# Performance work log

Measured on AMD Instinct MI355X. Metric: run time of the kernel, lower is better.

Reference implementation:

```python
import jax, jax.numpy as jnp
import numpy as np
import math

B, S, D, NH, HFF, E, K, C, L, V = 8, 256, 1024, 16, 2048, 8, 2, 10, 4, 32000
HD = D // NH
EPS = 1e-5


def _pos_encoding(max_len, d_model):
    pos = jnp.arange(max_len, dtype=jnp.float32)[:, None]
    div = jnp.exp(jnp.arange(0, d_model, 2, dtype=jnp.float32) * (-math.log(10000.0) / d_model))
    pe = jnp.zeros((max_len, d_model), dtype=jnp.float32)
    pe = pe.at[:, 0::2].set(jnp.sin(pos * div))
    pe = pe.at[:, 1::2].set(jnp.cos(pos * div))
    return pe[:, None, :]  # [max_len, 1, D], matching torch buffer layout


def _layernorm(x, g, b):
    mu = jnp.mean(x, axis=-1, keepdims=True)
    var = jnp.mean((x - mu) ** 2, axis=-1, keepdims=True)
    return (x - mu) * jax.lax.rsqrt(var + EPS) * g + b


def setup_inputs() -> dict:
    key = jax.random.key(0)
    ks = jax.random.split(key, 20)
    sc = lambda *shape: 0.02
    inp = {
        "src": jax.random.randint(ks[0], (B, S), 0, V, dtype=jnp.int32),
        "emb": jax.random.normal(ks[1], (V, D), jnp.float32) * 0.02,
        "in_proj_w": jax.random.normal(ks[2], (L, 3 * D, D), jnp.float32) * 0.02,
        "in_proj_b": jnp.zeros((L, 3 * D), jnp.float32),
        "out_w": jax.random.normal(ks[3], (L, D, D), jnp.float32) * 0.02,
        "out_b": jnp.zeros((L, D), jnp.float32),
        "ln1_g": jnp.ones((L, D), jnp.float32),
        "ln1_b": jnp.zeros((L, D), jnp.float32),
        "ln2_g": jnp.ones((L, D), jnp.float32),
        "ln2_b": jnp.zeros((L, D), jnp.float32),
        "gate_w": jax.random.normal(ks[4], (L, E, D), jnp.float32) * 0.02,
        "gate_b": jnp.zeros((L, E), jnp.float32),
        "w1": jax.random.normal(ks[5], (L, E, D, HFF), jnp.float32) * 0.02,
        "b1": jnp.zeros((L, E, HFF), jnp.float32),
        "w2": jax.random.normal(ks[6], (L, E, HFF, D), jnp.float32) * 0.02,
        "b2": jnp.zeros((L, E, D), jnp.float32),
        "cls_w": jax.random.normal(ks[7], (C, D), jnp.float32) * 0.02,
        "cls_b": jnp.zeros((C,), jnp.float32),
    }
    return inp


def _attention(x, ipw, ipb, ow, ob):
    # x: [B,S,D]
    qkv = x @ ipw.T + ipb  # [B,S,3D]
    q, k, v = jnp.split(qkv, 3, axis=-1)
    q = q.reshape(B, S, NH, HD)
    k = k.reshape(B, S, NH, HD)
    v = v.reshape(B, S, NH, HD)
    scores = jnp.einsum("bqhd,bkhd->bhqk", q, k) / math.sqrt(HD)
    attn = jax.nn.softmax(scores, axis=-1)
    o = jnp.einsum("bhqk,bkhd->bqhd", attn, v).reshape(B, S, D)
    return o @ ow.T + ob


def _moe(x, gw, gb, w1, b1, w2, b2):
    # x: [B,S,D]; gw: [E,D]; w1: [E,D,H]; w2: [E,H,D]
    t = x.reshape(B * S, D)
    logits = t @ gw.T + gb  # [T,E]
    topv, topi = jax.lax.top_k(logits, K)  # [T,K]
    weights = jax.nn.softmax(topv, axis=-1)  # [T,K]
    # dense expert compute (small E, compute-bound), combine via top-k gather
    h = jax.nn.relu(jnp.einsum("td,edh->teh", t, w1) + b1)  # [T,E,H]
    y = jnp.einsum("teh,ehd->ted", h, w2) + b2  # [T,E,D]
    sel = jnp.take_along_axis(y, topi[:, :, None], axis=1)  # [T,K,D]
    out = jnp.sum(sel * weights[:, :, None], axis=1)  # [T,D]
    return out.reshape(B, S, D), logits.reshape(B, S, E)


def reference(src, emb, in_proj_w, in_proj_b, out_w, out_b, ln1_g, ln1_b,
              ln2_g, ln2_b, gate_w, gate_b, w1, b1, w2, b2, cls_w, cls_b):
    x = emb[src] * math.sqrt(D)  # [B,S,D]
    pe = _pos_encoding(5000, D)  # [max_len,1,D]
    # faithful to original: pe indexed by batch dim (x.size(0)), broadcast over seq
    x = x + pe[:B]  # [B,1,D] -> broadcast [B,S,D]
    all_gates = []
    for l in range(in_proj_w.shape[0]):
        a = _attention(x, in_proj_w[l], in_proj_b[l], out_w[l], out_b[l])
        x = _layernorm(x + a, ln1_g[l], ln1_b[l])
        m, g = _moe(x, gate_w[l], gate_b[l], w1[l], b1[l], w2[l], b2[l])
        x = _layernorm(x + m, ln2_g[l], ln2_b[l])
        all_gates.append(g)
    pooled = jnp.mean(x, axis=1)  # [B,D]
    out = pooled @ cls_w.T + cls_b  # [B,C]
    return out, jnp.stack(all_gates)  # ([B,C], [L,B,S,E])
```

## Files before the change

### kernel.cpp

```cpp
#include <hip/hip_runtime.h>
#include <math.h>

#define TKN 2048
#define DIM 1024
#define NHEAD 16
#define HDIM 64
#define HFF 2048
#define NE 8
#define TOPK 2
#define NCLS 10
#define NLAYER 4
#define SEQ 256
#define BATCH 8

typedef __attribute__((ext_vector_type(8))) _Float16 f16x8;
typedef __attribute__((ext_vector_type(4))) float f32x4;
typedef __attribute__((ext_vector_type(16))) float f32x16;
typedef __attribute__((ext_vector_type(8))) unsigned short u16x8;

__device__ __forceinline__ unsigned short f2h(float v) {
  _Float16 h = (_Float16)v;
  return __builtin_bit_cast(unsigned short, h);
}
__device__ __forceinline__ void fsplit(float v, unsigned short& hi, unsigned short& lo) {
  _Float16 h = (_Float16)v;
  hi = __builtin_bit_cast(unsigned short, h);
  lo = f2h(v - (float)h);
}
__device__ __forceinline__ void split8(float4 f0, float4 f1, f16x8& h, f16x8& l) {
  float fv[8] = {f0.x, f0.y, f0.z, f0.w, f1.x, f1.y, f1.z, f1.w};
#pragma unroll
  for (int i = 0; i < 8; ++i) {
    _Float16 hh = (_Float16)fv[i];
    h[i] = hh;
    l[i] = (_Float16)(fv[i] - (float)hh);
  }
}

__device__ __forceinline__ void gload_lds16(const void* g, void* l) {
  __builtin_amdgcn_global_load_lds((__attribute__((address_space(1))) void*)g,
                                   (__attribute__((address_space(3))) void*)l,
                                   16, 0, 0);
}

__global__ __launch_bounds__(256) void k_embed(const int* __restrict__ src,
                                               const float* __restrict__ emb,
                                               float* __restrict__ x,
                                               unsigned short* __restrict__ xhi,
                                               unsigned short* __restrict__ xlo) {
  const int t = blockIdx.x;
  const int tid = threadIdx.x;
  const int b = t / SEQ;
  const int tok = src[t];
  const float* erow = emb + (size_t)tok * DIM;
  const size_t base = (size_t)t * DIM;
  const float cexp = -9.210340371976184f / 1024.0f;
#pragma unroll
  for (int j = 0; j < 4; ++j) {
    int d = tid + 256 * j;
    int i2 = d & ~1;
    float ang = (float)b * expf((float)i2 * cexp);
    float pe = (d & 1) ? cosf(ang) : sinf(ang);
    float v = erow[d] * 32.0f + pe;
    x[base + d] = v;
    fsplit(v, xhi[base + d], xlo[base + d]);
  }
}

template <bool LO>
__global__ __launch_bounds__(256) void k_cvt_split(const float* __restrict__ in,
                                                   unsigned short* __restrict__ ohi,
                                                   unsigned short* __restrict__ olo) {
  int i = blockIdx.x * 256 + threadIdx.x;
  float4 v = ((const float4*)in)[i];
  ushort4 h, l;
  fsplit(v.x, h.x, l.x); fsplit(v.y, h.y, l.y);
  fsplit(v.z, h.z, l.z); fsplit(v.w, h.w, l.w);
  ((ushort4*)ohi)[i] = h;
  if (LO) ((ushort4*)olo)[i] = l;
}

template <bool LO>
__global__ __launch_bounds__(256) void k_cvt_t2(const float* __restrict__ in,
                                                unsigned short* __restrict__ ohi,
                                                unsigned short* __restrict__ olo,
                                                int R, int Cc) {
  __shared__ float ts[64][33];
  const int t = threadIdx.x;
  const int c0 = blockIdx.x * 32, r0 = blockIdx.y * 64;
  const float* ip = in + (size_t)blockIdx.z * R * Cc;
  const size_t obase = (size_t)blockIdx.z * R * Cc;
  const int cc = t & 31, rr0 = t >> 5;
#pragma unroll
  for (int j = 0; j < 8; ++j)
    ts[rr0 + 8 * j][cc] = ip[(size_t)(r0 + rr0 + 8 * j) * Cc + c0 + cc];
  __syncthreads();
  const int c = t >> 3, rch = (t & 7) * 8;
  u16x8 hv, lv;
#pragma unroll
  for (int i = 0; i < 8; ++i) {
    unsigned short hi, lo;
    fsplit(ts[rch + i][c], hi, lo);
    hv[i] = hi; lv[i] = lo;
  }
  size_t o = obase + (size_t)(c0 + c) * R + r0 + rch;
  *(u16x8*)(ohi + o) = hv;
  if (LO) *(u16x8*)(olo + o) = lv;
}

template <int MODE, bool RELU, int OUTK, bool SPLIT>
__global__ __launch_bounds__(256) void k_mfma_gemm(
    const unsigned short* __restrict__ Ahi, const unsigned short* __restrict__ Alo,
    const unsigned short* __restrict__ Bhi, const unsigned short* __restrict__ Blo,
    const float* __restrict__ bias, void* __restrict__ out0, void* __restrict__ out1,
    int M, int N, int K,
    const int* __restrict__ slot_token, const int* __restrict__ offg) {
  constexpr int NP = SPLIT ? 2 : 1;
  __shared__ unsigned short U[2][NP][128 * 64];
  const int tid = threadIdx.x;
  const int w = tid >> 6, lane = tid & 63;
  const int bm = blockIdx.y * 128, bn = blockIdx.x * 128;
  int r0 = 0, rows = M, e = 0;
  if (MODE != 0) {
    e = blockIdx.z;
    r0 = offg[e];
    rows = offg[e + 1] - r0;
    if (bm >= rows) return;
  }
  const size_t bwb = (size_t)e * K * N;
  const float* biasq = bias + (size_t)e * N;

  const int lrow8 = lane >> 3;
  const int s = (lane & 7) ^ lrow8;
  const int chunk = (s & 3) * 8;
  const unsigned short* sp0[4];
  const unsigned short* sp1[4];
#pragma unroll
  for (int i = 0; i < 4; ++i) {
    int rloc = w * 32 + i * 8 + lrow8;
    int growA;
    if (MODE == 0) {
      growA = bm + rloc;
    } else {
      int rr = bm + rloc;
      if (rr >= rows) rr = rows - 1;
      growA = (MODE == 1) ? slot_token[r0 + rr] : (r0 + rr);
    }
    size_t aoff = (size_t)growA * K + chunk;
    size_t boff = bwb + (size_t)(bn + rloc) * K + chunk;
    if constexpr (SPLIT) {
      sp0[i] = (s < 4 ? Ahi : Alo) + aoff;
      sp1[i] = (s < 4 ? Bhi : Blo) + boff;
    } else {
      sp0[i] = (s < 4) ? (Ahi + aoff) : (Bhi + boff);
      sp1[i] = nullptr;
    }
  }

  f32x16 acc[2][2] = {};
  const int wr = w >> 1, wc = w & 1;
  const int l31 = lane & 31, kq = lane >> 5;
  const int sw = lane & 7;
  unsigned aof[2][2], bof[2][2];
#pragma unroll
  for (int mt = 0; mt < 2; ++mt)
#pragma unroll
    for (int kh = 0; kh < 2; ++kh)
      aof[mt][kh] = (unsigned)((wr * 64 + mt * 32 + l31) * 64 + (((kh * 2 + kq) ^ sw) * 8));
#pragma unroll
  for (int nt = 0; nt < 2; ++nt)
#pragma unroll
    for (int kh = 0; kh < 2; ++kh)
      bof[nt][kh] = (unsigned)((wc * 64 + nt * 32 + l31) * 64 + (((kh * 2 + kq) ^ sw) * 8));

#pragma unroll
  for (int i = 0; i < 4; ++i) {
    gload_lds16(sp0[i], &U[0][0][(w * 32 + i * 8) * 64]);
    sp0[i] += 32;
    if constexpr (SPLIT) {
      gload_lds16(sp1[i], &U[0][1][(w * 32 + i * 8) * 64]);
      sp1[i] += 32;
    }
  }

  const int NT = K / 32;
#pragma unroll 2
  for (int t = 0; t < NT; ++t) {
    const int cur = t & 1;
    if (t + 1 < NT) {
#pragma unroll
      for (int i = 0; i < 4; ++i) {
        gload_lds16(sp0[i], &U[cur ^ 1][0][(w * 32 + i * 8) * 64]);
        sp0[i] += 32;
        if constexpr (SPLIT) {
          gload_lds16(sp1[i], &U[cur ^ 1][1][(w * 32 + i * 8) * 64]);
          sp1[i] += 32;
        }
      }
      if constexpr (SPLIT)
        asm volatile("s_waitcnt vmcnt(8)" ::: "memory");
      else
        asm volatile("s_waitcnt vmcnt(4)" ::: "memory");
    } else {
      asm volatile("s_waitcnt vmcnt(0)" ::: "memory");
    }
    __builtin_amdgcn_s_barrier();

    f16x8 Ah[2][2], Bh[2][2], Al[2][2], Bl[2][2];
#pragma unroll
    for (int mt = 0; mt < 2; ++mt)
#pragma unroll
      for (int kh = 0; kh < 2; ++kh) {
        Ah[mt][kh] = *(const f16x8*)&U[cur][0][aof[mt][kh]];
        if constexpr (SPLIT) Al[mt][kh] = *(const f16x8*)&U[cur][0][aof[mt][kh] ^ 32];
      }
#pragma unroll
    for (int nt = 0; nt < 2; ++nt)
#pragma unroll
      for (int kh = 0; kh < 2; ++kh) {
        if constexpr (SPLIT) {
          Bh[nt][kh] = *(const f16x8*)&U[cur][1][bof[nt][kh]];
          Bl[nt][kh] = *(const f16x8*)&U[cur][1][bof[nt][kh] ^ 32];
        } else {
          Bh[nt][kh] = *(const f16x8*)&U[cur][0][bof[nt][kh] ^ 32];
        }
      }
#pragma unroll
    for (int mt = 0; mt < 2; ++mt)
#pragma unroll
      for (int nt = 0; nt < 2; ++nt)
#pragma unroll
        for (int kh = 0; kh < 2; ++kh) {
          acc[mt][nt] = __builtin_amdgcn_mfma_f32_32x32x16_f16(Ah[mt][kh], Bh[nt][kh], acc[mt][nt], 0, 0, 0);
          if constexpr (SPLIT) {
            acc[mt][nt] = __builtin_amdgcn_mfma_f32_32x32x16_f16(Ah[mt][kh], Bl[nt][kh], acc[mt][nt], 0, 0, 0);
            acc[mt][nt] = __builtin_amdgcn_mfma_f32_32x32x16_f16(Al[mt][kh], Bh[nt][kh], acc[mt][nt], 0, 0, 0);
          }
        }
    __builtin_amdgcn_s_barrier();
  }

  float bv[2];
#pragma unroll
  for (int nt = 0; nt < 2; ++nt) bv[nt] = biasq[bn + wc * 64 + nt * 32 + l31];

#pragma unroll
  for (int mt = 0; mt < 2; ++mt) {
#pragma unroll
    for (int reg = 0; reg < 16; ++reg) {
      int rloc = (reg & 3) + 8 * (reg >> 2) + 4 * kq;
      int rowg = bm + wr * 64 + mt * 32 + rloc;
      if (MODE != 0 && rowg >= rows) continue;
      size_t crow = (size_t)((MODE == 0) ? rowg : (r0 + rowg)) * N;
#pragma unroll
      for (int nt = 0; nt < 2; ++nt) {
        float v = acc[mt][nt][reg] + bv[nt];
        if (RELU) v = fmaxf(v, 0.f);
        size_t o = crow + bn + wc * 64 + nt * 32 + l31;
        if (OUTK == 0) {
          ((float*)out0)[o] = v;
        } else if (OUTK == 1) {
          ((unsigned short*)out0)[o] = f2h(v);
        } else {
          unsigned short hi, lo;
          fsplit(v, hi, lo);
          ((unsigned short*)out0)[o] = hi;
          ((unsigned short*)out1)[o] = lo;
        }
      }
    }
  }
}

__global__ __launch_bounds__(256) void k_attn(const float* __restrict__ qkv,
                                              unsigned short* __restrict__ ohi,
                                              unsigned short* __restrict__ olo) {
  __shared__ float ps[16][256];
  const int qt = blockIdx.x, hh = blockIdx.y, bb = blockIdx.z;
  const int tid = threadIdx.x, w = tid >> 6, lane = tid & 63;
  const int lr = lane & 15, lg = lane >> 4;
  const int t0 = bb * SEQ + qt * 16;

  f16x8 qh[2], ql[2];
#pragma unroll
  for (int kh = 0; kh < 2; ++kh) {
    const float* qb = qkv + (size_t)(t0 + lr) * (3 * DIM) + hh * 64 + kh * 32 + lg * 8;
    split8(*(const float4*)qb, *(const float4*)(qb + 4), qh[kh], ql[kh]);
  }
#pragma unroll
  for (int nt = 0; nt < 4; ++nt) {
    f16x8 kvh[2], kvl[2];
#pragma unroll
    for (int kh = 0; kh < 2; ++kh) {
      const float* kb = qkv + (size_t)(bb * SEQ + w * 64 + nt * 16 + lr) * (3 * DIM)
                        + DIM + hh * 64 + kh * 32 + lg * 8;
      split8(*(const float4*)kb, *(const float4*)(kb + 4), kvh[kh], kvl[kh]);
    }
    f32x4 a = {0.f, 0.f, 0.f, 0.f};
#pragma unroll
    for (int kh = 0; kh < 2; ++kh) {
      a = __builtin_amdgcn_mfma_f32_16x16x32_f16(qh[kh], kvh[kh], a, 0, 0, 0);
// ... 41 lines not shown
    }
  }
  float accs[4] = {a0, a1, a2, a3};
#pragma unroll
  for (int j = 0; j < 4; ++j) {
    size_t o = (size_t)(t0 + qi0 + 4 * j) * DIM + hh * 64 + d;
    fsplit(accs[j], ohi[o], olo[o]);
  }
}

__device__ __forceinline__ float block_reduce_sum(float v, float* red) {
  const int tid = threadIdx.x;
  red[tid] = v;
  __syncthreads();
  for (int s = 128; s > 0; s >>= 1) {
    if (tid < s) red[tid] += red[tid + s];
    __syncthreads();
  }
  float r = red[0];
  __syncthreads();
  return r;
}

__global__ __launch_bounds__(256) void k_add_ln_gate(const float* __restrict__ xin,
                                                     const float* __restrict__ add,
                                                     const float* __restrict__ g,
                                                     const float* __restrict__ bt,
                                                     const float* __restrict__ gw,
                                                     const float* __restrict__ gb,
                                                     float* __restrict__ xout,
                                                     unsigned short* __restrict__ xhi,
                                                     unsigned short* __restrict__ xlo,
                                                     float* __restrict__ gout,
                                                     int* __restrict__ topi,
                                                     float* __restrict__ topw) {
  __shared__ float red[256];
  __shared__ float pw[4][NE];
  __shared__ float lgs[NE];
  const int t = blockIdx.x, tid = threadIdx.x;
  const size_t base = (size_t)t * DIM;
  float v[4];
  float s = 0.f;
#pragma unroll
  for (int j = 0; j < 4; ++j) {
    int d = tid + 256 * j;
    v[j] = xin[base + d] + add[base + d];
    s += v[j];
  }
  float mean = block_reduce_sum(s, red) * (1.0f / DIM);
  float s2 = 0.f;
#pragma unroll
  for (int j = 0; j < 4; ++j) { float dv = v[j] - mean; s2 += dv * dv; }
  float var = block_reduce_sum(s2, red) * (1.0f / DIM);
  float rs = rsqrtf(var + 1e-5f);
  float o[4];
#pragma unroll
  for (int j = 0; j < 4; ++j) {
    int d = tid + 256 * j;
    o[j] = (v[j] - mean) * rs * g[d] + bt[d];
    xout[base + d] = o[j];
    fsplit(o[j], xhi[base + d], xlo[base + d]);
  }
  const int wv = tid >> 6, lane = tid & 63;
  float p[NE];
#pragma unroll
  for (int e = 0; e < NE; ++e) {
    float pe = 0.f;
#pragma unroll
    for (int j = 0; j < 4; ++j) pe += o[j] * gw[(size_t)e * DIM + tid + 256 * j];
    for (int m = 32; m; m >>= 1) pe += __shfl_xor(pe, m);
    p[e] = pe;
  }
  if (lane == 0) {
#pragma unroll
    for (int e = 0; e < NE; ++e) pw[wv][e] = p[e];
  }
  __syncthreads();
  if (tid < NE) {
    float l = pw[0][tid] + pw[1][tid] + pw[2][tid] + pw[3][tid] + gb[tid];
    gout[(size_t)t * NE + tid] = l;
    lgs[tid] = l;
  }
  __syncthreads();
  if (tid == 0) {
    int i0 = 0; float v0 = lgs[0];
    for (int i = 1; i < NE; ++i) if (lgs[i] > v0) { v0 = lgs[i]; i0 = i; }
    int i1 = -1; float v1 = -1e30f;
    for (int i = 0; i < NE; ++i) { if (i == i0) continue; if (lgs[i] > v1) { v1 = lgs[i]; i1 = i; } }
    float e1 = expf(v1 - v0);
    float w0 = 1.0f / (1.0f + e1);
    topi[2 * t] = i0; topi[2 * t + 1] = i1;
    topw[2 * t] = w0; topw[2 * t + 1] = e1 * w0;
  }
}

__global__ __launch_bounds__(512) void k_route(const int* __restrict__ topi,
                                               int* __restrict__ offg,
                                               int* __restrict__ slot_token,
                                               int* __restrict__ slot_of) {
  __shared__ int cnt_s[NE];
  __shared__ int off_s[NE + 1];
  const int tid = threadIdx.x;
  const int w = tid >> 6, lane = tid & 63;
  int c = 0;
  for (int i = lane; i < TKN * TOPK; i += 64) c += (topi[i] == w) ? 1 : 0;
  for (int m = 32; m; m >>= 1) c += __shfl_xor(c, m);
  if (lane == 0) cnt_s[w] = c;
  __syncthreads();
  if (tid == 0) {
    off_s[0] = 0;
    for (int e2 = 0; e2 < NE; ++e2) off_s[e2 + 1] = off_s[e2] + cnt_s[e2];
    for (int e2 = 0; e2 <= NE; ++e2) offg[e2] = off_s[e2];
  }
  __syncthreads();
  int base = off_s[w];
  for (int i0 = 0; i0 < TKN * TOPK; i0 += 64) {
    int i = i0 + lane;
    bool mm = (topi[i] == w);
    unsigned long long mask = __ballot(mm ? 1 : 0);
    int rank = __popcll(mask & ((1ull << lane) - 1ull));
    if (mm) {
      int slot = base + rank;
      slot_token[slot] = i >> 1;
      slot_of[i] = slot;
    }
    base += __popcll(mask);
  }
}

__global__ __launch_bounds__(256) void k_moe_combine_ln(const float* __restrict__ xin,
                                                        const float* __restrict__ y,
                                                        const float* __restrict__ topw,
                                                        const int* __restrict__ slot_of,
                                                        const float* __restrict__ g,
                                                        const float* __restrict__ bt,
                                                        float* __restrict__ xout,
                                                        unsigned short* __restrict__ xhi,
                                                        unsigned short* __restrict__ xlo) {
  __shared__ float red[256];
  const int t = blockIdx.x, tid = threadIdx.x;
  const float w0 = topw[2 * t], w1v = topw[2 * t + 1];
  const int s0 = slot_of[2 * t], s1 = slot_of[2 * t + 1];
  const size_t base = (size_t)t * DIM;
  float v[4];
  float s = 0.f;
#pragma unroll
  for (int j = 0; j < 4; ++j) {
    int d = tid + 256 * j;
    v[j] = xin[base + d] + w0 * y[(size_t)s0 * DIM + d] + w1v * y[(size_t)s1 * DIM + d];
    s += v[j];
  }
  float mean = block_reduce_sum(s, red) * (1.0f / DIM);
  float s2 = 0.f;
#pragma unroll
  for (int j = 0; j < 4; ++j) { float dv = v[j] - mean; s2 += dv * dv; }
  float var = block_reduce_sum(s2, red) * (1.0f / DIM);
  float rs = rsqrtf(var + 1e-5f);
#pragma unroll
  for (int j = 0; j < 4; ++j) {
// ... 28 lines not shown
  }
}

extern "C" void kernel_launch(void* const* d_in, const int* in_sizes, int n_in,
                              void* d_out, int out_size, void* d_ws, size_t ws_size,
                              hipStream_t stream) {
  const int*   src  = (const int*)  d_in[0];
  const float* emb  = (const float*)d_in[1];
  const float* ipw  = (const float*)d_in[2];
  const float* ipb  = (const float*)d_in[3];
  const float* ow   = (const float*)d_in[4];
  const float* ob   = (const float*)d_in[5];
  const float* ln1g = (const float*)d_in[6];
  const float* ln1b = (const float*)d_in[7];
  const float* ln2g = (const float*)d_in[8];
  const float* ln2b = (const float*)d_in[9];
  const float* gw   = (const float*)d_in[10];
  const float* gb   = (const float*)d_in[11];
  const float* w1   = (const float*)d_in[12];
  const float* b1   = (const float*)d_in[13];
  const float* w2   = (const float*)d_in[14];
  const float* b2   = (const float*)d_in[15];
  const float* cw   = (const float*)d_in[16];
  const float* cb   = (const float*)d_in[17];
  float* out = (float*)d_out;

  char* ws = (char*)d_ws;
  size_t off = 0;
  auto carve = [&](size_t bytes) -> void* {
    void* p = ws + off;
    off += (bytes + 255) & ~(size_t)255;
    return p;
  };
  float*          x     = (float*)carve((size_t)TKN * DIM * 4);
  unsigned short* xhi   = (unsigned short*)carve((size_t)TKN * DIM * 2);
  unsigned short* xlo   = (unsigned short*)carve((size_t)TKN * DIM * 2);
  char*           bufQ  = (char*)carve((size_t)2 * TKN * TOPK * HFF * 2);
  float*          qkv   = (float*)bufQ;
  unsigned short* h_hi  = (unsigned short*)bufQ;
  unsigned short* h_lo  = (unsigned short*)(bufQ + (size_t)TKN * TOPK * HFF * 2);
  unsigned short* at_hi = (unsigned short*)carve((size_t)TKN * DIM * 2);
  unsigned short* at_lo = (unsigned short*)carve((size_t)TKN * DIM * 2);
  char*           bufP  = (char*)carve((size_t)TKN * TOPK * DIM * 4);
  float*          proj  = (float*)bufP;
  float*          ybuf  = (float*)bufP;
  unsigned short* wq_hi = (unsigned short*)carve((size_t)3 * DIM * DIM * 2);
  unsigned short* wq_lo = (unsigned short*)carve((size_t)3 * DIM * DIM * 2);
  unsigned short* wo_hi = (unsigned short*)carve((size_t)DIM * DIM * 2);
  unsigned short* wo_lo = (unsigned short*)carve((size_t)DIM * DIM * 2);
  unsigned short* wt_hi = (unsigned short*)carve((size_t)NE * DIM * HFF * 2);
  unsigned short* wt_lo = (unsigned short*)carve((size_t)NE * DIM * HFF * 2);
  float* topw       = (float*)carve((size_t)TKN * TOPK * 4);
  int*   topi       = (int*)  carve((size_t)TKN * TOPK * 4);
  int*   slot_token = (int*)  carve((size_t)TKN * TOPK * 4);
  int*   slot_of    = (int*)  carve((size_t)TKN * TOPK * 4);
  int*   offg       = (int*)  carve(64);

  k_embed<<<TKN, 256, 0, stream>>>(src, emb, x, xhi, xlo);

  for (int l = 0; l < NLAYER; ++l) {
    const float* ipw_l = ipw + (size_t)l * 3 * DIM * DIM;
    const float* ow_l  = ow  + (size_t)l * DIM * DIM;
    const float* w1_l  = w1  + (size_t)l * NE * DIM * HFF;
    const float* w2_l  = w2  + (size_t)l * NE * HFF * DIM;
    const bool spd = (l < 3);
    const bool spm = (l < 2);

    if (spd) {
      k_cvt_split<true><<<(3 * DIM * DIM) / 1024, 256, 0, stream>>>(ipw_l, wq_hi, wq_lo);
      k_cvt_split<true><<<(DIM * DIM) / 1024, 256, 0, stream>>>(ow_l, wo_hi, wo_lo);
    } else {
      k_cvt_split<false><<<(3 * DIM * DIM) / 1024, 256, 0, stream>>>(ipw_l, wq_hi, wq_lo);
      k_cvt_split<false><<<(DIM * DIM) / 1024, 256, 0, stream>>>(ow_l, wo_hi, wo_lo);
    }
    if (spm)
      k_cvt_t2<true><<<dim3(HFF / 32, DIM / 64, NE), 256, 0, stream>>>(w1_l, wt_hi, wt_lo, DIM, HFF);
    else
      k_cvt_t2<false><<<dim3(HFF / 32, DIM / 64, NE), 256, 0, stream>>>(w1_l, wt_hi, wt_lo, DIM, HFF);

    if (spd)
      k_mfma_gemm<0, false, 0, true><<<dim3(3 * DIM / 128, TKN / 128), 256, 0, stream>>>(
          xhi, xlo, wq_hi, wq_lo, ipb + (size_t)l * 3 * DIM, qkv, nullptr, TKN, 3 * DIM, DIM, nullptr, nullptr);
    else
      k_mfma_gemm<0, false, 0, false><<<dim3(3 * DIM / 128, TKN / 128), 256, 0, stream>>>(
          xhi, xlo, wq_hi, wq_lo, ipb + (size_t)l * 3 * DIM, qkv, nullptr, TKN, 3 * DIM, DIM, nullptr, nullptr);

    k_attn<<<dim3(SEQ / 16, NHEAD, BATCH), 256, 0, stream>>>(qkv, at_hi, at_lo);

    if (spd)
      k_mfma_gemm<0, false, 0, true><<<dim3(DIM / 128, TKN / 128), 256, 0, stream>>>(
          at_hi, at_lo, wo_hi, wo_lo, ob + (size_t)l * DIM, proj, nullptr, TKN, DIM, DIM, nullptr, nullptr);
    else
      k_mfma_gemm<0, false, 0, false><<<dim3(DIM / 128, TKN / 128), 256, 0, stream>>>(
          at_hi, at_lo, wo_hi, wo_lo, ob + (size_t)l * DIM, proj, nullptr, TKN, DIM, DIM, nullptr, nullptr);

    k_add_ln_gate<<<TKN, 256, 0, stream>>>(x, proj, ln1g + l * DIM, ln1b + l * DIM,
                                           gw + (size_t)l * NE * DIM, gb + l * NE,
                                           x, xhi, xlo,
                                           out + NCLS * BATCH + (size_t)l * TKN * NE, topi, topw);
    k_route<<<1, 512, 0, stream>>>(topi, offg, slot_token, slot_of);

    if (spm)
      k_mfma_gemm<1, true, 2, true><<<dim3(HFF / 128, TKN * TOPK / 128, NE), 256, 0, stream>>>(
          xhi, xlo, wt_hi, wt_lo, b1 + (size_t)l * NE * HFF, h_hi, h_lo, 0, HFF, DIM, slot_token, offg);
    else
      k_mfma_gemm<1, true, 1, false><<<dim3(HFF / 128, TKN * TOPK / 128, NE), 256, 0, stream>>>(
          xhi, xlo, wt_hi, wt_lo, b1 + (size_t)l * NE * HFF, h_hi, nullptr, 0, HFF, DIM, slot_token, offg);

    if (spm)
      k_cvt_t2<true><<<dim3(DIM / 32, HFF / 64, NE), 256, 0, stream>>>(w2_l, wt_hi, wt_lo, HFF, DIM);
    else
      k_cvt_t2<false><<<dim3(DIM / 32, HFF / 64, NE), 256, 0, stream>>>(w2_l, wt_hi, wt_lo, HFF, DIM);

    if (spm)
      k_mfma_gemm<2, false, 0, true><<<dim3(DIM / 128, TKN * TOPK / 128, NE), 256, 0, stream>>>(
          h_hi, h_lo, wt_hi, wt_lo, b2 + (size_t)l * NE * DIM, ybuf, nullptr, 0, DIM, HFF, nullptr, offg);
    else
      k_mfma_gemm<2, false, 0, false><<<dim3(DIM / 128, TKN * TOPK / 128, NE), 256, 0, stream>>>(
          h_hi, h_lo, wt_hi, wt_lo, b2 + (size_t)l * NE * DIM, ybuf, nullptr, 0, DIM, HFF, nullptr, offg);

    k_moe_combine_ln<<<TKN, 256, 0, stream>>>(x, ybuf, topw, slot_of,
                                              ln2g + l * DIM, ln2b + l * DIM, x, xhi, xlo);
  }
  k_pool_cls<<<BATCH, 256, 0, stream>>>(x, cw, cb, out);
}
```

Measured before the change: 1.447 ms.

## Split MFMA GEMM tile across eight waves and merge weight conversion launches

The 128x128 MFMA GEMM block now runs 512 threads (8 waves), with each wave computing a 64x32 sub-tile instead of 64x64. Global-to-LDS loading and the wait counts are rebalanced to match. The aim is to cut per-wave accumulator registers and get more waves per CU to hide memory and LDS latency. In exchange, each wave reuses fragments less, so LDS reads per MFMA rise, and every k-step barrier now has to sync more waves. Separately, the two QKV and output-projection weight conversion kernels are fused into one launch with an index split.

```diff
diff --git a/kernel.cpp b/kernel.cpp
--- a/kernel.cpp
+++ b/kernel.cpp
@@ -68,16 +68,25 @@
 }
 
 template <bool LO>
-__global__ __launch_bounds__(256) void k_cvt_split(const float* __restrict__ in,
-                                                   unsigned short* __restrict__ ohi,
-                                                   unsigned short* __restrict__ olo) {
+__global__ __launch_bounds__(256) void k_cvt_split2(const float* __restrict__ inA,
+                                                    unsigned short* __restrict__ hA,
+                                                    unsigned short* __restrict__ lA,
+                                                    int n4A,
+                                                    const float* __restrict__ inB,
+                                                    unsigned short* __restrict__ hB,
+                                                    unsigned short* __restrict__ lB) {
   int i = blockIdx.x * 256 + threadIdx.x;
-  float4 v = ((const float4*)in)[i];
+  const float* in;
+  unsigned short *oh, *ol;
+  int j;
+  if (i < n4A) { in = inA; oh = hA; ol = lA; j = i; }
+  else         { in = inB; oh = hB; ol = lB; j = i - n4A; }
+  float4 v = ((const float4*)in)[j];
   ushort4 h, l;
   fsplit(v.x, h.x, l.x); fsplit(v.y, h.y, l.y);
   fsplit(v.z, h.z, l.z); fsplit(v.w, h.w, l.w);
-  ((ushort4*)ohi)[i] = h;
-  if (LO) ((ushort4*)olo)[i] = l;
+  ((ushort4*)oh)[j] = h;
+  if (LO) ((ushort4*)ol)[j] = l;
 }
 
 template <bool LO>
@@ -109,7 +118,7 @@
 }
 
 template <int MODE, bool RELU, int OUTK, bool SPLIT>
-__global__ __launch_bounds__(256) void k_mfma_gemm(
+__global__ __launch_bounds__(512, 4) void k_mfma_gemm(
     const unsigned short* __restrict__ Ahi, const unsigned short* __restrict__ Alo,
     const unsigned short* __restrict__ Bhi, const unsigned short* __restrict__ Blo,
     const float* __restrict__ bias, void* __restrict__ out0, void* __restrict__ out1,
@@ -133,11 +142,11 @@
   const int lrow8 = lane >> 3;
   const int s = (lane & 7) ^ lrow8;
   const int chunk = (s & 3) * 8;
-  const unsigned short* sp0[4];
-  const unsigned short* sp1[4];
-#pragma unroll
-  for (int i = 0; i < 4; ++i) {
-    int rloc = w * 32 + i * 8 + lrow8;
+  const unsigned short* sp0[2];
+  const unsigned short* sp1[2];
+#pragma unroll
+  for (int i = 0; i < 2; ++i) {
+    int rloc = w * 16 + i * 8 + lrow8;
     int growA;
     if (MODE == 0) {
       growA = bm + rloc;
@@ -157,28 +166,26 @@
     }
   }
 
-  f32x16 acc[2][2] = {};
-  const int wr = w >> 1, wc = w & 1;
+  f32x16 acc[2] = {};
+  const int wr = w >> 2, wc = w & 3;
   const int l31 = lane & 31, kq = lane >> 5;
-  const int sw = lane & 7;
-  unsigned aof[2][2], bof[2][2];
+  const int sw = l31 & 7;
+  unsigned aof[2][2], bof[2];
 #pragma unroll
   for (int mt = 0; mt < 2; ++mt)
 #pragma unroll
     for (int kh = 0; kh < 2; ++kh)
       aof[mt][kh] = (unsigned)((wr * 64 + mt * 32 + l31) * 64 + (((kh * 2 + kq) ^ sw) * 8));
 #pragma unroll
-  for (int nt = 0; nt < 2; ++nt)
-#pragma unroll
-    for (int kh = 0; kh < 2; ++kh)
-      bof[nt][kh] = (unsigned)((wc * 64 + nt * 32 + l31) * 64 + (((kh * 2 + kq) ^ sw) * 8));
-
-#pragma unroll
-  for (int i = 0; i < 4; ++i) {
-    gload_lds16(sp0[i], &U[0][0][(w * 32 + i * 8) * 64]);
+  for (int kh = 0; kh < 2; ++kh)
+    bof[kh] = (unsigned)((wc * 32 + l31) * 64 + (((kh * 2 + kq) ^ sw) * 8));
+
+#pragma unroll
+  for (int i = 0; i < 2; ++i) {
+    gload_lds16(sp0[i], &U[0][0][(w * 16 + i * 8) * 64]);
     sp0[i] += 32;
     if constexpr (SPLIT) {
-      gload_lds16(sp1[i], &U[0][1][(w * 32 + i * 8) * 64]);
+      gload_lds16(sp1[i], &U[0][1][(w * 16 + i * 8) * 64]);
       sp1[i] += 32;
     }
   }
@@ -189,61 +196,48 @@
     const int cur = t & 1;
     if (t + 1 < NT) {
 #pragma unroll
-      for (int i = 0; i < 4; ++i) {
-        gload_lds16(sp0[i], &U[cur ^ 1][0][(w * 32 + i * 8) * 64]);
+      for (int i = 0; i < 2; ++i) {
+        gload_lds16(sp0[i], &U[cur ^ 1][0][(w * 16 + i * 8) * 64]);
         sp0[i] += 32;
         if constexpr (SPLIT) {
-          gload_lds16(sp1[i], &U[cur ^ 1][1][(w * 32 + i * 8) * 64]);
+          gload_lds16(sp1[i], &U[cur ^ 1][1][(w * 16 + i * 8) * 64]);
           sp1[i] += 32;
         }
       }
       if constexpr (SPLIT)
-        asm volatile("s_waitcnt vmcnt(8)" ::: "memory");
+        asm volatile("s_waitcnt vmcnt(4)" ::: "memory");
       else
-        asm volatile("s_waitcnt vmcnt(4)" ::: "memory");
+        asm volatile("s_waitcnt vmcnt(2)" ::: "memory");
     } else {
       asm volatile("s_waitcnt vmcnt(0)" ::: "memory");
     }
     __builtin_amdgcn_s_barrier();
 
-    f16x8 Ah[2][2], Bh[2][2], Al[2][2], Bl[2][2];
-#pragma unroll
-    for (int mt = 0; mt < 2; ++mt)
-#pragma unroll
-      for (int kh = 0; kh < 2; ++kh) {
-        Ah[mt][kh] = *(const f16x8*)&U[cur][0][aof[mt][kh]];
-        if constexpr (SPLIT) Al[mt][kh] = *(const f16x8*)&U[cur][0][aof[mt][kh] ^ 32];
+#pragma unroll
+    for (int kh = 0; kh < 2; ++kh) {
+      f16x8 Ah0 = *(const f16x8*)&U[cur][0][aof[0][kh]];
+      f16x8 Ah1 = *(const f16x8*)&U[cur][0][aof[1][kh]];
+      if constexpr (SPLIT) {
+        f16x8 Bhv = *(const f16x8*)&U[cur][1][bof[kh]];
+        f16x8 Al0 = *(const f16x8*)&U[cur][0][aof[0][kh] ^ 32];
+        f16x8 Al1 = *(const f16x8*)&U[cur][0][aof[1][kh] ^ 32];
+        f16x8 Blv = *(const f16x8*)&U[cur][1][bof[kh] ^ 32];
+        acc[0] = __builtin_amdgcn_mfma_f32_32x32x16_f16(Ah0, Bhv, acc[0], 0, 0, 0);
+        acc[0] = __builtin_amdgcn_mfma_f32_32x32x16_f16(Ah0, Blv, acc[0], 0, 0, 0);
+        acc[0] = __builtin_amdgcn_mfma_f32_32x32x16_f16(Al0, Bhv, acc[0], 0, 0, 0);
+        acc[1] = __builtin_amdgcn_mfma_f32_32x32x16_f16(Ah1, Bhv, acc[1], 0, 0, 0);
+        acc[1] = __builtin_amdgcn_mfma_f32_32x32x16_f16(Ah1, Blv, acc[1], 0, 0, 0);
+        acc[1] = __builtin_amdgcn_mfma_f32_32x32x16_f16(Al1, Bhv, acc[1], 0, 0, 0);
+      } else {
+        f16x8 Bhv = *(const f16x8*)&U[cur][0][bof[kh] ^ 32];
+        acc[0] = __builtin_amdgcn_mfma_f32_32x32x16_f16(Ah0, Bhv, acc[0], 0, 0, 0);
+        acc[1] = __builtin_amdgcn_mfma_f32_32x32x16_f16(Ah1, Bhv, acc[1], 0, 0, 0);
       }
-#pragma unroll
-    for (int nt = 0; nt < 2; ++nt)
-#pragma unroll
-      for (int kh = 0; kh < 2; ++kh) {
-        if constexpr (SPLIT) {
-          Bh[nt][kh] = *(const f16x8*)&U[cur][1][bof[nt][kh]];
-          Bl[nt][kh] = *(const f16x8*)&U[cur][1][bof[nt][kh] ^ 32];
-        } else {
-          Bh[nt][kh] = *(const f16x8*)&U[cur][0][bof[nt][kh] ^ 32];
-        }
-      }
-#pragma unroll
-    for (int mt = 0; mt < 2; ++mt)
-#pragma unroll
-      for (int nt = 0; nt < 2; ++nt)
-#pragma unroll
-        for (int kh = 0; kh < 2; ++kh) {
-          acc[mt][nt] = __builtin_amdgcn_mfma_f32_32x32x16_f16(Ah[mt][kh], Bh[nt][kh], acc[mt][nt], 0, 0, 0);
-          if constexpr (SPLIT) {
-            acc[mt][nt] = __builtin_amdgcn_mfma_f32_32x32x16_f16(Ah[mt][kh], Bl[nt][kh], acc[mt][nt], 0, 0, 0);
-            acc[mt][nt] = __builtin_amdgcn_mfma_f32_32x32x16_f16(Al[mt][kh], Bh[nt][kh], acc[mt][nt], 0, 0, 0);
-          }
-        }
+    }
     __builtin_amdgcn_s_barrier();
   }
 
-  float bv[2];
-#pragma unroll
-  for (int nt = 0; nt < 2; ++nt) bv[nt] = biasq[bn + wc * 64 + nt * 32 + l31];
-
+  const float bv = biasq[bn + wc * 32 + l31];
 #pragma unroll
   for (int mt = 0; mt < 2; ++mt) {
 #pragma unroll
@@ -252,21 +246,18 @@
       int rowg = bm + wr * 64 + mt * 32 + rloc;
       if (MODE != 0 && rowg >= rows) continue;
       size_t crow = (size_t)((MODE == 0) ? rowg : (r0 + rowg)) * N;
-#pragma unroll
-      for (int nt = 0; nt < 2; ++nt) {
-        float v = acc[mt][nt][reg] + bv[nt];
-        if (RELU) v = fmaxf(v, 0.f);
-        size_t o = crow + bn + wc * 64 + nt * 32 + l31;
-        if (OUTK == 0) {
-          ((float*)out0)[o] = v;
-        } else if (OUTK == 1) {
-          ((unsigned short*)out0)[o] = f2h(v);
-        } else {
-          unsigned short hi, lo;
-          fsplit(v, hi, lo);
-          ((unsigned short*)out0)[o] = hi;
-          ((unsigned short*)out1)[o] = lo;
-        }
+      float v = acc[mt][reg] + bv;
+      if (RELU) v = fmaxf(v, 0.f);
+      size_t o = crow + bn + wc * 32 + l31;
+      if (OUTK == 0) {
+        ((float*)out0)[o] = v;
+      } else if (OUTK == 1) {
+        ((unsigned short*)out0)[o] = f2h(v);
+      } else {
+        unsigned short hi, lo;
+        fsplit(v, hi, lo);
+        ((unsigned short*)out0)[o] = hi;
+        ((unsigned short*)out1)[o] = lo;
       }
     }
   }
@@ -587,6 +578,8 @@
 
   k_embed<<<TKN, 256, 0, stream>>>(src, emb, x, xhi, xlo);
 
+  const int n4wq = 3 * DIM * DIM / 4;
+
   for (int l = 0; l < NLAYER; ++l) {
     const float* ipw_l = ipw + (size_t)l * 3 * DIM * DIM;
     const float* ow_l  = ow  + (size_t)l * DIM * DIM;
@@ -595,32 +588,31 @@
     const bool spd = (l < 3);
     const bool spm = (l < 2);
 
-    if (spd) {
-      k_cvt_split<true><<<(3 * DIM * DIM) / 1024, 256, 0, stream>>>(ipw_l, wq_hi, wq_lo);
-      k_cvt_split<true><<<(DIM * DIM) / 1024, 256, 0, stream>>>(ow_l, wo_hi, wo_lo);
-    } else {
-      k_cvt_split<false><<<(3 * DIM * DIM) / 1024, 256, 0, stream>>>(ipw_l, wq_hi, wq_lo);
-      k_cvt_split<false><<<(DIM * DIM) / 1024, 256, 0, stream>>>(ow_l, wo_hi, wo_lo);
-    }
+    if (spd)
+      k_cvt_split2<true><<<(4 * DIM * DIM) / 1024, 256, 0, stream>>>(
+          ipw_l, wq_hi, wq_lo, n4wq, ow_l, wo_hi, wo_lo);
+    else
+      k_cvt_split2<false><<<(4 * DIM * DIM) / 1024, 256, 0, stream>>>(
+          ipw_l, wq_hi, wq_lo, n4wq, ow_l, wo_hi, wo_lo);
     if (spm)
       k_cvt_t2<true><<<dim3(HFF / 32, DIM / 64, NE), 256, 0, stream>>>(w1_l, wt_hi, wt_lo, DIM, HFF);
     else
       k_cvt_t2<false><<<dim3(HFF / 32, DIM / 64, NE), 256, 0, stream>>>(w1_l, wt_hi, wt_lo, DIM, HFF);
 
     if (spd)
-      k_mfma_gemm<0, false, 0, true><<<dim3(3 * DIM / 128, TKN / 128), 256, 0, stream>>>(
+      k_mfma_gemm<0, false, 0, true><<<dim3(3 * DIM / 128, TKN / 128), 512, 0, stream>>>(
           xhi, xlo, wq_hi, wq_lo, ipb + (size_t)l * 3 * DIM, qkv, nullptr, TKN, 3 * DIM, DIM, nullptr, nullptr);
     else
-      k_mfma_gemm<0, false, 0, false><<<dim3(3 * DIM / 128, TKN / 128), 256, 0, stream>>>(
+      k_mfma_gemm<0, false, 0, false><<<dim3(3 * DIM / 128, TKN / 128), 512, 0, stream>>>(
           xhi, xlo, wq_hi, wq_lo, ipb + (size_t)l * 3 * DIM, qkv, nullptr, TKN, 3 * DIM, DIM, nullptr, nullptr);
 
     k_attn<<<dim3(SEQ / 16, NHEAD, BATCH), 256, 0, stream>>>(qkv, at_hi, at_lo);
 
     if (spd)
-      k_mfma_gemm<0, false, 0, true><<<dim3(DIM / 128, TKN / 128), 256, 0, stream>>>(
+      k_mfma_gemm<0, false, 0, true><<<dim3(DIM / 128, TKN / 128), 512, 0, stream>>>(
           at_hi, at_lo, wo_hi, wo_lo, ob + (size_t)l * DIM, proj, nullptr, TKN, DIM, DIM, nullptr, nullptr);
     else
-      k_mfma_gemm<0, false, 0, false><<<dim3(DIM / 128, TKN / 128), 256, 0, stream>>>(
+      k_mfma_gemm<0, false, 0, false><<<dim3(DIM / 128, TKN / 128), 512, 0, stream>>>(
           at_hi, at_lo, wo_hi, wo_lo, ob + (size_t)l * DIM, proj, nullptr, TKN, DIM, DIM, nullptr, nullptr);
 
     k_add_ln_gate<<<TKN, 256, 0, stream>>>(x, proj, ln1g + l * DIM, ln1b + l * DIM,
@@ -630,10 +622,10 @@
     k_route<<<1, 512, 0, stream>>>(topi, offg, slot_token, slot_of);
 
     if (spm)
-      k_mfma_gemm<1, true, 2, true><<<dim3(HFF / 128, TKN * TOPK / 128, NE), 256, 0, stream>>>(
+      k_mfma_gemm<1, true, 2, true><<<dim3(HFF / 128, TKN * TOPK / 128, NE), 512, 0, stream>>>(
           xhi, xlo, wt_hi, wt_lo, b1 + (size_t)l * NE * HFF, h_hi, h_lo, 0, HFF, DIM, slot_token, offg);
     else
-      k_mfma_gemm<1, true, 1, false><<<dim3(HFF / 128, TKN * TOPK / 128, NE), 256, 0, stream>>>(
+      k_mfma_gemm<1, true, 1, false><<<dim3(HFF / 128, TKN * TOPK / 128, NE), 512, 0, stream>>>(
           xhi, xlo, wt_hi, wt_lo, b1 + (size_t)l * NE * HFF, h_hi, nullptr, 0, HFF, DIM, slot_token, offg);
 
     if (spm)
@@ -642,10 +634,10 @@
       k_cvt_t2<false><<<dim3(DIM / 32, HFF / 64, NE), 256, 0, stream>>>(w2_l, wt_hi, wt_lo, HFF, DIM);
 
     if (spm)
-      k_mfma_gemm<2, false, 0, true><<<dim3(DIM / 128, TKN * TOPK / 128, NE), 256, 0, stream>>>(
+      k_mfma_gemm<2, false, 0, true><<<dim3(DIM / 128, TKN * TOPK / 128, NE), 512, 0, stream>>>(
           h_hi, h_lo, wt_hi, wt_lo, b2 + (size_t)l * NE * DIM, ybuf, nullptr, 0, DIM, HFF, nullptr, offg);
     else
-      k_mfma_gemm<2, false, 0, false><<<dim3(DIM / 128, TKN * TOPK / 128, NE), 256, 0, stream>>>(
+      k_mfma_gemm<2, false, 0, false><<<dim3(DIM / 128, TKN * TOPK / 128, NE), 512, 0, stream>>>(
           h_hi, h_lo, wt_hi, wt_lo, b2 + (size_t)l * NE * DIM, ybuf, nullptr, 0, DIM, HFF, nullptr, offg);
 
     k_moe_combine_ln<<<TKN, 256, 0, stream>>>(x, ybuf, topw, slot_of,
```

New measurement: 1.483 ms. 2.5% more time.

## Replace route kernel with atomic slot assignment and merge weight conversion launches

Applied to the files above, without the earlier changes.

The single-block routing kernel is removed. The gate kernel now claims expert slots directly with atomicAdd into fixed-capacity per-expert regions, and the counters are zeroed in the embed kernel. The qkv/out weight conversions and the w1/w2 transpose conversions are each merged into one launch, with separate buffers so w2 no longer waits on the first expert GEMM. This cuts the kernel launch count and removes a serial one-block routing step. In exchange, slot order becomes nondeterministic, buffers grow to NE*CAP, and the expert grids launch more blocks that exit early.

```diff
diff --git a/kernel.cpp b/kernel.cpp
--- a/kernel.cpp
+++ b/kernel.cpp
@@ -12,6 +12,7 @@
 #define NLAYER 4
 #define SEQ 256
 #define BATCH 8
+#define CAP 2048
 
 typedef __attribute__((ext_vector_type(8))) _Float16 f16x8;
 typedef __attribute__((ext_vector_type(4))) float f32x4;
@@ -47,9 +48,11 @@
                                                const float* __restrict__ emb,
                                                float* __restrict__ x,
                                                unsigned short* __restrict__ xhi,
-                                               unsigned short* __restrict__ xlo) {
+                                               unsigned short* __restrict__ xlo,
+                                               int* __restrict__ cnt_all) {
   const int t = blockIdx.x;
   const int tid = threadIdx.x;
+  if (t == 0 && tid < NLAYER * NE) cnt_all[tid] = 0;
   const int b = t / SEQ;
   const int tok = src[t];
   const float* erow = emb + (size_t)tok * DIM;
@@ -68,32 +71,56 @@
 }
 
 template <bool LO>
-__global__ __launch_bounds__(256) void k_cvt_split(const float* __restrict__ in,
-                                                   unsigned short* __restrict__ ohi,
-                                                   unsigned short* __restrict__ olo) {
+__global__ __launch_bounds__(256) void k_cvt_split2(const float* __restrict__ inA,
+                                                    unsigned short* __restrict__ hA,
+                                                    unsigned short* __restrict__ lA,
+                                                    int n4A,
+                                                    const float* __restrict__ inB,
+                                                    unsigned short* __restrict__ hB,
+                                                    unsigned short* __restrict__ lB) {
   int i = blockIdx.x * 256 + threadIdx.x;
-  float4 v = ((const float4*)in)[i];
+  const float* in;
+  unsigned short *oh, *ol;
+  int j;
+  if (i < n4A) { in = inA; oh = hA; ol = lA; j = i; }
+  else         { in = inB; oh = hB; ol = lB; j = i - n4A; }
+  float4 v = ((const float4*)in)[j];
   ushort4 h, l;
   fsplit(v.x, h.x, l.x); fsplit(v.y, h.y, l.y);
   fsplit(v.z, h.z, l.z); fsplit(v.w, h.w, l.w);
-  ((ushort4*)ohi)[i] = h;
-  if (LO) ((ushort4*)olo)[i] = l;
+  ((ushort4*)oh)[j] = h;
+  if (LO) ((ushort4*)ol)[j] = l;
 }
 
 template <bool LO>
-__global__ __launch_bounds__(256) void k_cvt_t2(const float* __restrict__ in,
-                                                unsigned short* __restrict__ ohi,
-                                                unsigned short* __restrict__ olo,
-                                                int R, int Cc) {
+__global__ __launch_bounds__(256) void k_cvt_t2_w12(
+    const float* __restrict__ w1, unsigned short* __restrict__ o1h, unsigned short* __restrict__ o1l,
+    const float* __restrict__ w2, unsigned short* __restrict__ o2h, unsigned short* __restrict__ o2l) {
   __shared__ float ts[64][33];
   const int t = threadIdx.x;
-  const int c0 = blockIdx.x * 32, r0 = blockIdx.y * 64;
-  const float* ip = in + (size_t)blockIdx.z * R * Cc;
-  const size_t obase = (size_t)blockIdx.z * R * Cc;
+  const int z = blockIdx.z;
+  const float* in;
+  unsigned short *ohi, *olo;
+  int R, Cc, bx, by;
+  if (z < NE) {
+    in = w1 + (size_t)z * DIM * HFF;
+    ohi = o1h + (size_t)z * DIM * HFF;
+    olo = o1l + (size_t)z * DIM * HFF;
+    R = DIM; Cc = HFF; bx = blockIdx.x; by = blockIdx.y;
+  } else {
+    int e = z - NE;
+    in = w2 + (size_t)e * HFF * DIM;
+    ohi = o2h + (size_t)e * HFF * DIM;
+    olo = o2l + (size_t)e * HFF * DIM;
+    R = HFF; Cc = DIM;
+    int id = blockIdx.y * 64 + blockIdx.x;
+    bx = id & 31; by = id >> 5;
+  }
+  const int c0 = bx * 32, r0 = by * 64;
   const int cc = t & 31, rr0 = t >> 5;
 #pragma unroll
   for (int j = 0; j < 8; ++j)
-    ts[rr0 + 8 * j][cc] = ip[(size_t)(r0 + rr0 + 8 * j) * Cc + c0 + cc];
+    ts[rr0 + 8 * j][cc] = in[(size_t)(r0 + rr0 + 8 * j) * Cc + c0 + cc];
   __syncthreads();
   const int c = t >> 3, rch = (t & 7) * 8;
   u16x8 hv, lv;
@@ -103,7 +130,7 @@
     fsplit(ts[rch + i][c], hi, lo);
     hv[i] = hi; lv[i] = lo;
   }
-  size_t o = obase + (size_t)(c0 + c) * R + r0 + rch;
+  size_t o = (size_t)(c0 + c) * R + r0 + rch;
   *(u16x8*)(ohi + o) = hv;
   if (LO) *(u16x8*)(olo + o) = lv;
 }
@@ -114,7 +141,7 @@
     const unsigned short* __restrict__ Bhi, const unsigned short* __restrict__ Blo,
     const float* __restrict__ bias, void* __restrict__ out0, void* __restrict__ out1,
     int M, int N, int K,
-    const int* __restrict__ slot_token, const int* __restrict__ offg) {
+    const int* __restrict__ slot_token, const int* __restrict__ cnt) {
   constexpr int NP = SPLIT ? 2 : 1;
   __shared__ unsigned short U[2][NP][128 * 64];
   const int tid = threadIdx.x;
@@ -123,8 +150,8 @@
   int r0 = 0, rows = M, e = 0;
   if (MODE != 0) {
     e = blockIdx.z;
-    r0 = offg[e];
-    rows = offg[e + 1] - r0;
+    r0 = e * CAP;
+    rows = cnt[e];
     if (bm >= rows) return;
   }
   const size_t bwb = (size_t)e * K * N;
@@ -160,7 +187,7 @@
   f32x16 acc[2][2] = {};
   const int wr = w >> 1, wc = w & 1;
   const int l31 = lane & 31, kq = lane >> 5;
-  const int sw = lane & 7;
+  const int sw = l31 & 7;
   unsigned aof[2][2], bof[2][2];
 #pragma unroll
   for (int mt = 0; mt < 2; ++mt)
@@ -374,7 +401,9 @@
                                                      unsigned short* __restrict__ xhi,
                                                      unsigned short* __restrict__ xlo,
                                                      float* __restrict__ gout,
-                                                     int* __restrict__ topi,
+                                                     int* __restrict__ cnt,
+                                                     int* __restrict__ slot_token,
+                                                     int* __restrict__ slot_of,
                                                      float* __restrict__ topw) {
   __shared__ float red[256];
   __shared__ float pw[4][NE];
@@ -431,42 +460,13 @@
     for (int i = 0; i < NE; ++i) { if (i == i0) continue; if (lgs[i] > v1) { v1 = lgs[i]; i1 = i; } }
     float e1 = expf(v1 - v0);
     float w0 = 1.0f / (1.0f + e1);
-    topi[2 * t] = i0; topi[2 * t + 1] = i1;
     topw[2 * t] = w0; topw[2 * t + 1] = e1 * w0;
-  }
-}
-
-__global__ __launch_bounds__(512) void k_route(const int* __restrict__ topi,
-                                               int* __restrict__ offg,
-                                               int* __restrict__ slot_token,
-                                               int* __restrict__ slot_of) {
-  __shared__ int cnt_s[NE];
-  __shared__ int off_s[NE + 1];
-  const int tid = threadIdx.x;
-  const int w = tid >> 6, lane = tid & 63;
-  int c = 0;
-  for (int i = lane; i < TKN * TOPK; i += 64) c += (topi[i] == w) ? 1 : 0;
-  for (int m = 32; m; m >>= 1) c += __shfl_xor(c, m);
-  if (lane == 0) cnt_s[w] = c;
-  __syncthreads();
-  if (tid == 0) {
-    off_s[0] = 0;
-    for (int e2 = 0; e2 < NE; ++e2) off_s[e2 + 1] = off_s[e2] + cnt_s[e2];
-    for (int e2 = 0; e2 <= NE; ++e2) offg[e2] = off_s[e2];
-  }
-  __syncthreads();
-  int base = off_s[w];
-  for (int i0 = 0; i0 < TKN * TOPK; i0 += 64) {
-    int i = i0 + lane;
-    bool mm = (topi[i] == w);
-    unsigned long long mask = __ballot(mm ? 1 : 0);
-    int rank = __popcll(mask & ((1ull << lane) - 1ull));
-    if (mm) {
-      int slot = base + rank;
-      slot_token[slot] = i >> 1;
-      slot_of[i] = slot;
-    }
-    base += __popcll(mask);
+    int idx0 = atomicAdd(&cnt[i0], 1);
+    int idx1 = atomicAdd(&cnt[i1], 1);
+    slot_token[i0 * CAP + idx0] = t;
+    slot_token[i1 * CAP + idx1] = t;
+    slot_of[2 * t] = i0 * CAP + idx0;
+    slot_of[2 * t + 1] = i1 * CAP + idx1;
   }
 }
 
@@ -561,51 +561,54 @@
     off += (bytes + 255) & ~(size_t)255;
     return p;
   };
-  float*          x     = (float*)carve((size_t)TKN * DIM * 4);
-  unsigned short* xhi   = (unsigned short*)carve((size_t)TKN * DIM * 2);
-  unsigned short* xlo   = (unsigned short*)carve((size_t)TKN * DIM * 2);
-  char*           bufQ  = (char*)carve((size_t)2 * TKN * TOPK * HFF * 2);
-  float*          qkv   = (float*)bufQ;
-  unsigned short* h_hi  = (unsigned short*)bufQ;
-  unsigned short* h_lo  = (unsigned short*)(bufQ + (size_t)TKN * TOPK * HFF * 2);
-  unsigned short* at_hi = (unsigned short*)carve((size_t)TKN * DIM * 2);
-  unsigned short* at_lo = (unsigned short*)carve((size_t)TKN * DIM * 2);
-  char*           bufP  = (char*)carve((size_t)TKN * TOPK * DIM * 4);
-  float*          proj  = (float*)bufP;
-  float*          ybuf  = (float*)bufP;
-  unsigned short* wq_hi = (unsigned short*)carve((size_t)3 * DIM * DIM * 2);
-  unsigned short* wq_lo = (unsigned short*)carve((size_t)3 * DIM * DIM * 2);
-  unsigned short* wo_hi = (unsigned short*)carve((size_t)DIM * DIM * 2);
-  unsigned short* wo_lo = (unsigned short*)carve((size_t)DIM * DIM * 2);
-  unsigned short* wt_hi = (unsigned short*)carve((size_t)NE * DIM * HFF * 2);
-  unsigned short* wt_lo = (unsigned short*)carve((size_t)NE * DIM * HFF * 2);
+  float*          x      = (float*)carve((size_t)TKN * DIM * 4);
+  unsigned short* xhi    = (unsigned short*)carve((size_t)TKN * DIM * 2);
+  unsigned short* xlo    = (unsigned short*)carve((size_t)TKN * DIM * 2);
+  float*          qkv    = (float*)carve((size_t)TKN * 3 * DIM * 4);
+  unsigned short* h_hi   = (unsigned short*)carve((size_t)NE * CAP * HFF * 2);
+  unsigned short* h_lo   = (unsigned short*)carve((size_t)NE * CAP * HFF * 2);
+  unsigned short* at_hi  = (unsigned short*)carve((size_t)TKN * DIM * 2);
+  unsigned short* at_lo  = (unsigned short*)carve((size_t)TKN * DIM * 2);
+  float*          proj   = (float*)carve((size_t)TKN * DIM * 4);
+  float*          ybuf   = (float*)carve((size_t)NE * CAP * DIM * 4);
+  unsigned short* wq_hi  = (unsigned short*)carve((size_t)3 * DIM * DIM * 2);
+  unsigned short* wq_lo  = (unsigned short*)carve((size_t)3 * DIM * DIM * 2);
+  unsigned short* wo_hi  = (unsigned short*)carve((size_t)DIM * DIM * 2);
+  unsigned short* wo_lo  = (unsigned short*)carve((size_t)DIM * DIM * 2);
+  unsigned short* wt1_hi = (unsigned short*)carve((size_t)NE * DIM * HFF * 2);
+  unsigned short* wt1_lo = (unsigned short*)carve((size_t)NE * DIM * HFF * 2);
+  unsigned short* wt2_hi = (unsigned short*)carve((size_t)NE * DIM * HFF * 2);
+  unsigned short* wt2_lo = (unsigned short*)carve((size_t)NE * DIM * HFF * 2);
   float* topw       = (float*)carve((size_t)TKN * TOPK * 4);
-  int*   topi       = (int*)  carve((size_t)TKN * TOPK * 4);
-  int*   slot_token = (int*)  carve((size_t)TKN * TOPK * 4);
+  int*   slot_token = (int*)  carve((size_t)NE * CAP * 4);
   int*   slot_of    = (int*)  carve((size_t)TKN * TOPK * 4);
-  int*   offg       = (int*)  carve(64);
-
-  k_embed<<<TKN, 256, 0, stream>>>(src, emb, x, xhi, xlo);
+  int*   cnt        = (int*)  carve((size_t)NLAYER * NE * 4);
+
+  k_embed<<<TKN, 256, 0, stream>>>(src, emb, x, xhi, xlo, cnt);
+
+  const int n4wq = 3 * DIM * DIM / 4;
 
   for (int l = 0; l < NLAYER; ++l) {
     const float* ipw_l = ipw + (size_t)l * 3 * DIM * DIM;
     const float* ow_l  = ow  + (size_t)l * DIM * DIM;
     const float* w1_l  = w1  + (size_t)l * NE * DIM * HFF;
     const float* w2_l  = w2  + (size_t)l * NE * HFF * DIM;
+    int* cnt_l = cnt + l * NE;
     const bool spd = (l < 3);
     const bool spm = (l < 2);
 
-    if (spd) {
-      k_cvt_split<true><<<(3 * DIM * DIM) / 1024, 256, 0, stream>>>(ipw_l, wq_hi, wq_lo);
-      k_cvt_split<true><<<(DIM * DIM) / 1024, 256, 0, stream>>>(ow_l, wo_hi, wo_lo);
-    } else {
-      k_cvt_split<false><<<(3 * DIM * DIM) / 1024, 256, 0, stream>>>(ipw_l, wq_hi, wq_lo);
-      k_cvt_split<false><<<(DIM * DIM) / 1024, 256, 0, stream>>>(ow_l, wo_hi, wo_lo);
-    }
+    if (spd)
+      k_cvt_split2<true><<<(4 * DIM * DIM) / 1024, 256, 0, stream>>>(
+          ipw_l, wq_hi, wq_lo, n4wq, ow_l, wo_hi, wo_lo);
+    else
+      k_cvt_split2<false><<<(4 * DIM * DIM) / 1024, 256, 0, stream>>>(
+          ipw_l, wq_hi, wq_lo, n4wq, ow_l, wo_hi, wo_lo);
     if (spm)
-      k_cvt_t2<true><<<dim3(HFF / 32, DIM / 64, NE), 256, 0, stream>>>(w1_l, wt_hi, wt_lo, DIM, HFF);
+      k_cvt_t2_w12<true><<<dim3(64, 16, 2 * NE), 256, 0, stream>>>(
+          w1_l, wt1_hi, wt1_lo, w2_l, wt2_hi, wt2_lo);
     else
-      k_cvt_t2<false><<<dim3(HFF / 32, DIM / 64, NE), 256, 0, stream>>>(w1_l, wt_hi, wt_lo, DIM, HFF);
+      k_cvt_t2_w12<false><<<dim3(64, 16, 2 * NE), 256, 0, stream>>>(
+          w1_l, wt1_hi, wt1_lo, w2_l, wt2_hi, wt2_lo);
 
     if (spd)
       k_mfma_gemm<0, false, 0, true><<<dim3(3 * DIM / 128, TKN / 128), 256, 0, stream>>>(
@@ -626,27 +629,22 @@
     k_add_ln_gate<<<TKN, 256, 0, stream>>>(x, proj, ln1g + l * DIM, ln1b + l * DIM,
                                            gw + (size_t)l * NE * DIM, gb + l * NE,
                                            x, xhi, xlo,
-                                           out + NCLS * BATCH + (size_t)l * TKN * NE, topi, topw);
-    k_route<<<1, 512, 0, stream>>>(topi, offg, slot_token, slot_of);
+                                           out + NCLS * BATCH + (size_t)l * TKN * NE,
+                                           cnt_l, slot_token, slot_of, topw);
 
     if (spm)
-      k_mfma_gemm<1, true, 2, true><<<dim3(HFF / 128, TKN * TOPK / 128, NE), 256, 0, stream>>>(
-          xhi, xlo, wt_hi, wt_lo, b1 + (size_t)l * NE * HFF, h_hi, h_lo, 0, HFF, DIM, slot_token, offg);
+      k_mfma_gemm<1, true, 2, true><<<dim3(HFF / 128, CAP / 128, NE), 256, 0, stream>>>(
+          xhi, xlo, wt1_hi, wt1_lo, b1 + (size_t)l * NE * HFF, h_hi, h_lo, 0, HFF, DIM, slot_token, cnt_l);
     else
-      k_mfma_gemm<1, true, 1, false><<<dim3(HFF / 128, TKN * TOPK / 128, NE), 256, 0, stream>>>(
-          xhi, xlo, wt_hi, wt_lo, b1 + (size_t)l * NE * HFF, h_hi, nullptr, 0, HFF, DIM, slot_token, offg);
+      k_mfma_gemm<1, true, 1, false><<<dim3(HFF / 128, CAP / 128, NE), 256, 0, stream>>>(
+          xhi, xlo, wt1_hi, wt1_lo, b1 + (size_t)l * NE * HFF, h_hi, nullptr, 0, HFF, DIM, slot_token, cnt_l);
 
     if (spm)
-      k_cvt_t2<true><<<dim3(DIM / 32, HFF / 64, NE), 256, 0, stream>>>(w2_l, wt_hi, wt_lo, HFF, DIM);
+      k_mfma_gemm<2, false, 0, true><<<dim3(DIM / 128, CAP / 128, NE), 256, 0, stream>>>(
+          h_hi, h_lo, wt2_hi, wt2_lo, b2 + (size_t)l * NE * DIM, ybuf, nullptr, 0, DIM, HFF, nullptr, cnt_l);
     else
-      k_cvt_t2<false><<<dim3(DIM / 32, HFF / 64, NE), 256, 0, stream>>>(w2_l, wt_hi, wt_lo, HFF, DIM);
-
-    if (spm)
-      k_mfma_gemm<2, false, 0, true><<<dim3(DIM / 128, TKN * TOPK / 128, NE), 256, 0, stream>>>(
-          h_hi, h_lo, wt_hi, wt_lo, b2 + (size_t)l * NE * DIM, ybuf, nullptr, 0, DIM, HFF, nullptr, offg);
-    else
-      k_mfma_gemm<2, false, 0, false><<<dim3(DIM / 128, TKN * TOPK / 128, NE), 256, 0, stream>>>(
-          h_hi, h_lo, wt_hi, wt_lo, b2 + (size_t)l * NE * DIM, ybuf, nullptr, 0, DIM, HFF, nullptr, offg);
+      k_mfma_gemm<2, false, 0, false><<<dim3(DIM / 128, CAP / 128, NE), 256, 0, stream>>>(
+          h_hi, h_lo, wt2_hi, wt2_lo, b2 + (size_t)l * NE * DIM, ybuf, nullptr, 0, DIM, HFF, nullptr, cnt_l);
 
     k_moe_combine_ln<<<TKN, 256, 0, stream>>>(x, ybuf, topw, slot_of,
                                               ln2g + l * DIM, ln2b + l * DIM, x, xhi, xlo);
```

Result: slower. 1.618 ms (+11.8%).
